# Kernel optimization log

Measured on AMD Instinct MI355X. Metric: run time of the kernel, lower is better.

The kernel has to match this reference:

```python
import jax, jax.numpy as jnp
import numpy as np

DIL = 1  # dilation


def setup_inputs() -> dict:
    key = jax.random.key(0)
    k0, k1, k2, k3 = jax.random.split(key, 4)
    B, Cin, Cout, K, L, NR = 16, 256, 256, 3, 4096, 5
    x = jax.random.normal(k0, (B, Cin, L), jnp.float32)
    # kaiming-uniform-ish scale for conv kernels
    base_kernels = jax.random.normal(k1, (NR, Cout, Cin, K), jnp.float32) * (1.0 / np.sqrt(Cin * K))
    base_biases = jax.random.normal(k2, (NR, Cout), jnp.float32) * (1.0 / np.sqrt(Cin * K))
    # controller: Linear(Cin*K -> NR) followed by softmax over rules
    ctrl_w = jax.random.normal(k3, (Cin * K, NR), jnp.float32) * (1.0 / np.sqrt(Cin * K))
    ctrl_b = jnp.zeros((NR,), jnp.float32)
    return {"x": x, "base_kernels": base_kernels, "base_biases": base_biases,
            "ctrl_w": ctrl_w, "ctrl_b": ctrl_b}


def reference(x, base_kernels, base_biases, ctrl_w, ctrl_b):
    NR, Cout, Cin, K = base_kernels.shape
    B, _, L = x.shape
    pad = (K - 1) * DIL
    px = jnp.pad(x, ((0, 0), (0, 0), (pad, 0)))  # causal left pad -> (B, Cin, L+pad)

    # patches: padded_x.unfold(dim=2, size=K, step=1)[:, :, :L] -> (B, Cin, L, K)
    patches = jnp.stack([px[:, :, k:k + L] for k in range(K)], axis=-1)
    patches = patches.transpose(0, 2, 1, 3).reshape(B, L, Cin * K)  # (B, L, Cin*K)

    # controller -> normalized firing strengths (B, L, NR)
    fr = jax.nn.softmax(patches @ ctrl_w + ctrl_b, axis=-1)

    # all n_rules causal convs in one grouped-as-batched-output conv
    rhs = base_kernels.reshape(NR * Cout, Cin, K)
    conv = jax.lax.conv_general_dilated(
        px, rhs, window_strides=(1,), padding=[(0, 0)],
        rhs_dilation=(DIL,), dimension_numbers=("NCH", "OIH", "NCH"))  # (B, NR*Cout, L)
    conv = conv.reshape(B, NR, Cout, L) + base_biases[None, :, :, None]

    # weighted sum over experts: sum_n fr[b,l,n] * conv[b,n,o,l]
    return jnp.einsum("bnol,bln->bol", conv, fr)
```

## Files before the change

### kernel.cpp

```cpp
#include <hip/hip_runtime.h>
#include <hip/hip_bf16.h>

typedef __attribute__((ext_vector_type(4))) float floatx4;
typedef __attribute__((ext_vector_type(8))) short shortx8;

#define NB   16
#define CIN  256
#define COUT 256
#define KW   3
#define LL   4096
#define LLP  4098
#define NR   5
#define QK   768
#define NP   65536

static __device__ __forceinline__ unsigned short bf16bits(float f) {
    __hip_bfloat16 h = __float2bfloat16(f);
    return __builtin_bit_cast(unsigned short, h);
}

static __device__ __forceinline__ void gload16(const void* g, void* l) {
    __builtin_amdgcn_global_load_lds(
        (const __attribute__((address_space(1))) void*)g,
        (__attribute__((address_space(3))) void*)l, 16, 0, 0);
}

__global__ void k_tfr(const float* __restrict__ x, const float* __restrict__ bk,
                      const float* __restrict__ cw,
                      __hip_bfloat16* __restrict__ wb, __hip_bfloat16* __restrict__ wc,
                      __hip_bfloat16* __restrict__ xt) {
    __shared__ float t[64][65];
    int l0 = blockIdx.x * 64, b = blockIdx.y;
    int bid = blockIdx.y * 64 + blockIdx.x;
    int tid = threadIdx.x;
    int r16 = tid >> 4, q16 = tid & 15;

    #pragma unroll
    for (int jj = 0; jj < 4; ++jj) {
        int i = bid * 1024 + jj * 256 + tid;
        if (i < NR * COUT * QK) {
            int m = i / QK, qq = i % QK;
            int o = (m / 80) * 16 + (m & 15);
            int r = (m % 80) / 16;
            int k = qq >> 8, cin = qq & 255;
            wb[i] = __float2bfloat16(bk[((r * COUT + o) * CIN + cin) * KW + k]);
        }
    }
    if (bid < 48) {
        int row = bid, cin = tid;
        int kh = row >> 4, r = row & 15;
        float v = (r < NR) ? cw[(cin * 3 + kh) * NR + r] : 0.f;
        wc[row * 256 + cin] = __float2bfloat16(v);
    }
    {
        int i0 = bid * 256 + tid;
        if (i0 < NB * 2 * CIN) {
            int bb = i0 >> 9, rr = i0 & 511;
            xt[(size_t)bb * LLP * CIN + rr] = __float2bfloat16(0.f);
        }
    }

    for (int ch = 0; ch < 4; ++ch) {
        __syncthreads();
        #pragma unroll
        for (int pass = 0; pass < 4; ++pass) {
            int cin = pass * 16 + r16;
            float4 v = *(const float4*)&x[((size_t)(b * CIN + ch * 64 + cin)) * LL + l0 + q16 * 4];
            t[q16 * 4 + 0][cin] = v.x;
            t[q16 * 4 + 1][cin] = v.y;
            t[q16 * 4 + 2][cin] = v.z;
            t[q16 * 4 + 3][cin] = v.w;
        }
        __syncthreads();
        #pragma unroll
        for (int pass = 0; pass < 4; ++pass) {
            int lr = pass * 16 + r16;
            int c4 = q16 * 4;
            ushort4 u;
            u.x = bf16bits(t[lr][c4 + 0]);
            u.y = bf16bits(t[lr][c4 + 1]);
            u.z = bf16bits(t[lr][c4 + 2]);
            u.w = bf16bits(t[lr][c4 + 3]);
            *(ushort4*)&xt[((size_t)(b * LLP + 2 + l0 + lr)) * CIN + ch * 64 + c4] = u;
        }
    }
}

#define XBUF  8256
#define WBUF2 9216
#define WOFF2 16512
__global__ __launch_bounds__(256, 2)
void k_conv(const __hip_bfloat16* __restrict__ xt, const __hip_bfloat16* __restrict__ wb,
            const __hip_bfloat16* __restrict__ wc, const float* __restrict__ bias,
            const float* __restrict__ cbv, float* __restrict__ out) {
    __shared__ __align__(16) short lds[2 * XBUF + 2 * WBUF2];
    __shared__ float bs[80];

    int g = blockIdx.x;
    int pt = ((g >> 7) << 3) | (g & 7);
    int y  = (g >> 3) & 15;
    int p0 = pt * 256;
    int m0 = y * 80, o0 = y * 16;
    int b = p0 >> 12, l0 = p0 & (LL - 1);
    int tid = threadIdx.x;
    int lane = tid & 63, wn = tid >> 6;
    int quad = lane >> 4, l16 = lane & 15;

    const __hip_bfloat16* xb = xt + (size_t)b * (LLP * CIN);

    if (tid < 80) bs[tid] = bias[(tid >> 4) * COUT + o0 + (tid & 15)];
    float cbl[NR];
    #pragma unroll
    for (int n = 0; n < NR; ++n) cbl[n] = cbv[n];

    int xchk[5];
    #pragma unroll
    for (int j = 0; j < 4; ++j) xchk[j] = j * 256 + tid;
    xchk[4] = 968 + lane;
    int xsrc[5];
    #pragma unroll
    for (int j = 0; j < 5; ++j) {
        int c = xchk[j];
        int row = c >> 2, cs = c & 3;
        int cg = cs ^ ((row >> 1) & 3);
        xsrc[j] = (l0 + row) * CIN + cg * 8;
    }
    int wchk[5];
    #pragma unroll
    for (int j = 0; j < 4; ++j) wchk[j] = j * 256 + tid;
    wchk[4] = 1024 + (tid & 127);
    const __hip_bfloat16* wp[5];
    #pragma unroll
    for (int j = 0; j < 5; ++j) {
        int c = wchk[j];
        int s = c >> 2, cs = c & 3;
        int cg = cs ^ ((s >> 1) & 3);
        int kh = s / 96, mp = s - kh * 96;
        wp[j] = (mp < 80) ? wb + ((m0 + mp) * QK + kh * 256 + cg * 8)
                          : wc + ((kh * 16 + mp - 80) * 256 + cg * 8);
    }

    int boff[3][4], aoff[3][6];
    #pragma unroll
    for (int kh = 0; kh < 3; ++kh) {
        #pragma unroll
        for (int nf = 0; nf < 4; ++nf) {
            int row = wn * 64 + nf * 16 + l16 + kh;
            boff[kh][nf] = row * 32 + (quad ^ ((row >> 1) & 3)) * 8;
        }
        #pragma unroll
        for (int mf = 0; mf < 6; ++mf) {
            int s = kh * 96 + mf * 16 + l16;
            aoff[kh][mf] = s * 32 + (quad ^ ((s >> 1) & 3)) * 8;
        }
    }

    floatx4 acc[6][4];
    #pragma unroll
    for (int mf = 0; mf < 6; ++mf)
        #pragma unroll
        for (int nf = 0; nf < 4; ++nf)
            acc[mf][nf] = (floatx4){0.f, 0.f, 0.f, 0.f};

    auto stage = [&](int buf, int ph) {
        short* BX = &lds[buf * XBUF];
        const __hip_bfloat16* xp = xb + ph * 32;
        #pragma unroll
        for (int j = 0; j < 5; ++j)
            gload16(xp + xsrc[j], BX + xchk[j] * 8);
        short* BW = &lds[WOFF2 + buf * WBUF2];
        #pragma unroll
        for (int j = 0; j < 5; ++j)
            gload16(wp[j] + ph * 32, BW + wchk[j] * 8);
    };

    auto compute = [&](int buf) {
        const short* X = &lds[buf * XBUF];
        const short* W = &lds[WOFF2 + buf * WBUF2];
        #pragma unroll
        for (int kh = 0; kh < 3; ++kh) {
            shortx8 bfrag[4], afrag[6];
            #pragma unroll
            for (int nf = 0; nf < 4; ++nf)
                bfrag[nf] = *(const shortx8*)&X[boff[kh][nf]];
            #pragma unroll
            for (int mf = 0; mf < 6; ++mf)
                afrag[mf] = *(const shortx8*)&W[aoff[kh][mf]];
            #pragma unroll
            for (int mf = 0; mf < 6; ++mf)
                #pragma unroll
                for (int nf = 0; nf < 4; ++nf)
                    acc[mf][nf] = __builtin_amdgcn_mfma_f32_16x16x32_bf16(
                        afrag[mf], bfrag[nf], acc[mf][nf], 0, 0, 0);
        }
    };

    stage(0, 0);
    __syncthreads();
    #pragma unroll
    for (int ph = 0; ph < 8; ++ph) {
        if (ph < 7) stage((ph + 1) & 1, ph + 1);
        compute(ph & 1);
        __syncthreads();
    }

    float* scf = (float*)lds;
    int pb = wn * 576;
    #pragma unroll
    for (int nf = 0; nf < 4; ++nf) {
        int pp = pb + (nf * 16 + l16) * 9;
        if (quad == 0) {
            scf[pp + 0] = acc[5][nf][0];
            scf[pp + 1] = acc[5][nf][1];
            scf[pp + 2] = acc[5][nf][2];
            scf[pp + 3] = acc[5][nf][3];
        } else if (quad == 1) {
            scf[pp + 4] = acc[5][nf][0];
        }
    }
    __syncthreads();

    #pragma unroll
    for (int nf = 0; nf < 4; ++nf) {
        int colp = wn * 64 + nf * 16 + l16;
        int pp = pb + (nf * 16 + l16) * 9;
        float l2[NR];
        #pragma unroll
        for (int n = 0; n < NR; ++n) l2[n] = scf[pp + n] + cbl[n];
        float mx = l2[0];
        #pragma unroll
        for (int n = 1; n < NR; ++n) mx = fmaxf(mx, l2[n]);
        float e[NR], s = 0.f;
        #pragma unroll
        for (int n = 0; n < NR; ++n) { e[n] = __expf(l2[n] - mx); s += e[n]; }
        float inv = 1.f / s;
        float f0 = e[0] * inv, f1 = e[1] * inv, f2 = e[2] * inv, f3 = e[3] * inv, f4 = e[4] * inv;
        #pragma unroll
        for (int j = 0; j < 4; ++j) {
            int olo = quad * 4 + j;
            float v = f0 * (acc[0][nf][j] + bs[0 * 16 + olo])
                    + f1 * (acc[1][nf][j] + bs[1 * 16 + olo])
                    + f2 * (acc[2][nf][j] + bs[2 * 16 + olo])
                    + f3 * (acc[3][nf][j] + bs[3 * 16 + olo])
                    + f4 * (acc[4][nf][j] + bs[4 * 16 + olo]);
            out[((size_t)(b * COUT + o0 + olo)) * LL + l0 + colp] = v;
        }
    }
}

extern "C" void kernel_launch(void* const* d_in, const int* in_sizes, int n_in,
                              void* d_out, int out_size, void* d_ws, size_t ws_size,
                              hipStream_t stream) {
    const float* x  = (const float*)d_in[0];
    const float* bk = (const float*)d_in[1];
    const float* bb = (const float*)d_in[2];
    const float* cw = (const float*)d_in[3];
    const float* cb = (const float*)d_in[4];
    float* out = (float*)d_out;

    char* ws = (char*)d_ws;
    __hip_bfloat16* xt = (__hip_bfloat16*)ws;
    __hip_bfloat16* wb = (__hip_bfloat16*)(ws + 33570816);
    __hip_bfloat16* wc = (__hip_bfloat16*)(ws + 33570816 + 1966080);

    k_tfr<<<dim3(LL / 64, NB), dim3(256), 0, stream>>>(x, bk, cw, wb, wc, xt);
    k_conv<<<dim3(NP / 256 * (COUT / 16)), dim3(256), 0, stream>>>(xt, wb, wc, bb, cb, out);
}
```

Before: 253.9 us.

## Switch conv GEMM to 32x32x16 MFMA with larger 1024-position, 512-thread tiles

The conv kernel moves from 16x16x32 bf16 MFMA fragments to 32x32x16 fragments. Each block now covers 1024 positions with 8 waves instead of 256 positions with 4 waves, and the K loop runs as 16 phases of 16 channels instead of 8 phases of 32. The LDS layout drops the XOR swizzle in favour of a split-half chunk layout, and the epilogue is remapped to the new accumulator layout. This aims to reuse weight tiles across more positions and get more MMA throughput per fragment load. The cost is more phases and barriers, and possible LDS bank conflicts without the swizzle.

```diff
diff --git a/kernel.cpp b/kernel.cpp
--- a/kernel.cpp
+++ b/kernel.cpp
@@ -1,7 +1,7 @@
 #include <hip/hip_runtime.h>
 #include <hip/hip_bf16.h>
 
-typedef __attribute__((ext_vector_type(4))) float floatx4;
+typedef __attribute__((ext_vector_type(16))) float floatx16;
 typedef __attribute__((ext_vector_type(8))) short shortx8;
 
 #define NB   16
@@ -86,25 +86,25 @@
     }
 }
 
-#define XBUF  8256
-#define WBUF2 9216
-#define WOFF2 16512
-__global__ __launch_bounds__(256, 2)
+#define XCH   2052
+#define WCH2  576
+#define WBASE 4104
+__global__ __launch_bounds__(512, 2)
 void k_conv(const __hip_bfloat16* __restrict__ xt, const __hip_bfloat16* __restrict__ wb,
             const __hip_bfloat16* __restrict__ wc, const float* __restrict__ bias,
             const float* __restrict__ cbv, float* __restrict__ out) {
-    __shared__ __align__(16) short lds[2 * XBUF + 2 * WBUF2];
+    __shared__ __align__(16) short lds[(2 * XCH + 2 * WCH2) * 8];
     __shared__ float bs[80];
 
     int g = blockIdx.x;
     int pt = ((g >> 7) << 3) | (g & 7);
     int y  = (g >> 3) & 15;
-    int p0 = pt * 256;
+    int p0 = pt * 1024;
     int m0 = y * 80, o0 = y * 16;
     int b = p0 >> 12, l0 = p0 & (LL - 1);
     int tid = threadIdx.x;
     int lane = tid & 63, wn = tid >> 6;
-    int quad = lane >> 4, l16 = lane & 15;
+    int col = lane & 31, half = lane >> 5;
 
     const __hip_bfloat16* xb = xt + (size_t)b * (LLP * CIN);
 
@@ -113,117 +113,95 @@
     #pragma unroll
     for (int n = 0; n < NR; ++n) cbl[n] = cbv[n];
 
-    int xchk[5];
-    #pragma unroll
-    for (int j = 0; j < 4; ++j) xchk[j] = j * 256 + tid;
-    xchk[4] = 968 + lane;
-    int xsrc[5];
+    const int xbase[5] = {0, 512, 1024, 1536, 1540};
+    int xoff[5];
     #pragma unroll
     for (int j = 0; j < 5; ++j) {
-        int c = xchk[j];
-        int row = c >> 2, cs = c & 3;
-        int cg = cs ^ ((row >> 1) & 3);
-        xsrc[j] = (l0 + row) * CIN + cg * 8;
-    }
-    int wchk[5];
-    #pragma unroll
-    for (int j = 0; j < 4; ++j) wchk[j] = j * 256 + tid;
-    wchk[4] = 1024 + (tid & 127);
-    const __hip_bfloat16* wp[5];
-    #pragma unroll
-    for (int j = 0; j < 5; ++j) {
-        int c = wchk[j];
-        int s = c >> 2, cs = c & 3;
-        int cg = cs ^ ((s >> 1) & 3);
+        int c = xbase[j] + tid;
+        int h = c / 1026, row = c % 1026;
+        xoff[j] = (l0 + row) * CIN + h * 8;
+    }
+    const __hip_bfloat16* wptr[2];
+    #pragma unroll
+    for (int j = 0; j < 2; ++j) {
+        int c = (j == 0) ? tid : 64 + tid;
+        int h = c / 288, s = c % 288;
         int kh = s / 96, mp = s - kh * 96;
-        wp[j] = (mp < 80) ? wb + ((m0 + mp) * QK + kh * 256 + cg * 8)
-                          : wc + ((kh * 16 + mp - 80) * 256 + cg * 8);
-    }
-
-    int boff[3][4], aoff[3][6];
-    #pragma unroll
-    for (int kh = 0; kh < 3; ++kh) {
-        #pragma unroll
-        for (int nf = 0; nf < 4; ++nf) {
-            int row = wn * 64 + nf * 16 + l16 + kh;
-            boff[kh][nf] = row * 32 + (quad ^ ((row >> 1) & 3)) * 8;
-        }
-        #pragma unroll
-        for (int mf = 0; mf < 6; ++mf) {
-            int s = kh * 96 + mf * 16 + l16;
-            aoff[kh][mf] = s * 32 + (quad ^ ((s >> 1) & 3)) * 8;
-        }
-    }
-
-    floatx4 acc[6][4];
-    #pragma unroll
-    for (int mf = 0; mf < 6; ++mf)
+        wptr[j] = (mp < 80) ? wb + ((m0 + mp) * QK + kh * 256 + h * 8)
+                            : wc + ((kh * 16 + mp - 80) * 256 + h * 8);
+    }
+
+    int bbS = (half * 1026 + wn * 128 + col) * 8;
+    int aaS = (half * 288 + col) * 8;
+
+    floatx16 acc[3][4];
+    #pragma unroll
+    for (int mf = 0; mf < 3; ++mf)
         #pragma unroll
         for (int nf = 0; nf < 4; ++nf)
-            acc[mf][nf] = (floatx4){0.f, 0.f, 0.f, 0.f};
+            acc[mf][nf] = (floatx16)(0.f);
 
     auto stage = [&](int buf, int ph) {
-        short* BX = &lds[buf * XBUF];
-        const __hip_bfloat16* xp = xb + ph * 32;
+        short* BX = &lds[buf * XCH * 8];
+        const __hip_bfloat16* xp = xb + ph * 16;
         #pragma unroll
         for (int j = 0; j < 5; ++j)
-            gload16(xp + xsrc[j], BX + xchk[j] * 8);
-        short* BW = &lds[WOFF2 + buf * WBUF2];
-        #pragma unroll
-        for (int j = 0; j < 5; ++j)
-            gload16(wp[j] + ph * 32, BW + wchk[j] * 8);
+            gload16(xp + xoff[j], BX + (xbase[j] + wn * 64) * 8);
+        short* BW = &lds[(WBASE + buf * WCH2) * 8];
+        gload16(wptr[0] + ph * 16, BW + (wn * 64) * 8);
+        gload16(wptr[1] + ph * 16, BW + (64 + wn * 64) * 8);
     };
 
     auto compute = [&](int buf) {
-        const short* X = &lds[buf * XBUF];
-        const short* W = &lds[WOFF2 + buf * WBUF2];
+        const short* X = &lds[buf * XCH * 8];
+        const short* W = &lds[(WBASE + buf * WCH2) * 8];
         #pragma unroll
         for (int kh = 0; kh < 3; ++kh) {
-            shortx8 bfrag[4], afrag[6];
+            shortx8 af[3], bf[4];
+            #pragma unroll
+            for (int mf = 0; mf < 3; ++mf)
+                af[mf] = *(const shortx8*)&W[aaS + (kh * 96 + mf * 32) * 8];
             #pragma unroll
             for (int nf = 0; nf < 4; ++nf)
-                bfrag[nf] = *(const shortx8*)&X[boff[kh][nf]];
+                bf[nf] = *(const shortx8*)&X[bbS + (nf * 32 + kh) * 8];
             #pragma unroll
-            for (int mf = 0; mf < 6; ++mf)
-                afrag[mf] = *(const shortx8*)&W[aoff[kh][mf]];
-            #pragma unroll
-            for (int mf = 0; mf < 6; ++mf)
+            for (int mf = 0; mf < 3; ++mf)
                 #pragma unroll
                 for (int nf = 0; nf < 4; ++nf)
-                    acc[mf][nf] = __builtin_amdgcn_mfma_f32_16x16x32_bf16(
-                        afrag[mf], bfrag[nf], acc[mf][nf], 0, 0, 0);
+                    acc[mf][nf] = __builtin_amdgcn_mfma_f32_32x32x16_bf16(
+                        af[mf], bf[nf], acc[mf][nf], 0, 0, 0);
         }
     };
 
     stage(0, 0);
     __syncthreads();
     #pragma unroll
-    for (int ph = 0; ph < 8; ++ph) {
-        if (ph < 7) stage((ph + 1) & 1, ph + 1);
+    for (int ph = 0; ph < 16; ++ph) {
+        if (ph < 15) stage((ph + 1) & 1, ph + 1);
         compute(ph & 1);
         __syncthreads();
     }
 
     float* scf = (float*)lds;
-    int pb = wn * 576;
+    int sbase = wn * 128 * 6;
     #pragma unroll
     for (int nf = 0; nf < 4; ++nf) {
-        int pp = pb + (nf * 16 + l16) * 9;
-        if (quad == 0) {
-            scf[pp + 0] = acc[5][nf][0];
-            scf[pp + 1] = acc[5][nf][1];
-            scf[pp + 2] = acc[5][nf][2];
-            scf[pp + 3] = acc[5][nf][3];
-        } else if (quad == 1) {
-            scf[pp + 4] = acc[5][nf][0];
+        int pp = sbase + (nf * 32 + col) * 6;
+        if (half == 0) {
+            scf[pp + 0] = acc[2][nf][8];
+            scf[pp + 1] = acc[2][nf][9];
+            scf[pp + 2] = acc[2][nf][10];
+            scf[pp + 3] = acc[2][nf][11];
+        } else {
+            scf[pp + 4] = acc[2][nf][8];
         }
     }
     __syncthreads();
 
     #pragma unroll
     for (int nf = 0; nf < 4; ++nf) {
-        int colp = wn * 64 + nf * 16 + l16;
-        int pp = pb + (nf * 16 + l16) * 9;
+        int colp = wn * 128 + nf * 32 + col;
+        int pp = sbase + (nf * 32 + col) * 6;
         float l2[NR];
         #pragma unroll
         for (int n = 0; n < NR; ++n) l2[n] = scf[pp + n] + cbl[n];
@@ -236,13 +214,13 @@
         float inv = 1.f / s;
         float f0 = e[0] * inv, f1 = e[1] * inv, f2 = e[2] * inv, f3 = e[3] * inv, f4 = e[4] * inv;
         #pragma unroll
-        for (int j = 0; j < 4; ++j) {
-            int olo = quad * 4 + j;
-            float v = f0 * (acc[0][nf][j] + bs[0 * 16 + olo])
-                    + f1 * (acc[1][nf][j] + bs[1 * 16 + olo])
-                    + f2 * (acc[2][nf][j] + bs[2 * 16 + olo])
-                    + f3 * (acc[3][nf][j] + bs[3 * 16 + olo])
-                    + f4 * (acc[4][nf][j] + bs[4 * 16 + olo]);
+        for (int j = 0; j < 8; ++j) {
+            int olo = (j & 3) + 8 * (j >> 2) + 4 * half;
+            float v = f0 * (acc[0][nf][j]     + bs[ 0 + olo])
+                    + f1 * (acc[0][nf][j + 8] + bs[16 + olo])
+                    + f2 * (acc[1][nf][j]     + bs[32 + olo])
+                    + f3 * (acc[1][nf][j + 8] + bs[48 + olo])
+                    + f4 * (acc[2][nf][j]     + bs[64 + olo]);
             out[((size_t)(b * COUT + o0 + olo)) * LL + l0 + colp] = v;
         }
     }
@@ -264,5 +242,5 @@
     __hip_bfloat16* wc = (__hip_bfloat16*)(ws + 33570816 + 1966080);
 
     k_tfr<<<dim3(LL / 64, NB), dim3(256), 0, stream>>>(x, bk, cw, wb, wc, xt);
-    k_conv<<<dim3(NP / 256 * (COUT / 16)), dim3(256), 0, stream>>>(xt, wb, wc, bb, cb, out);
-}
+    k_conv<<<dim3(NP / 1024 * (COUT / 16)), dim3(512), 0, stream>>>(xt, wb, wc, bb, cb, out);
+}
```

Measured after the change: 349.5 us. 1.38x slower.
